# Optimization experiments

Measured on AMD Instinct MI355X. Metric: run time of the kernel, lower is better.

The kernel has to match this reference:

```python
import jax, jax.numpy as jnp
import numpy as np

N_NODES = 50000
N_EDGES = 800000
IN_F = 128
OUT_F = 128
EDGE_F = 6


def setup_inputs() -> dict:
    key = jax.random.key(0)
    k1, k2, k3, k4, k5, k6, k7 = jax.random.split(key, 7)
    nodeFeatures = jax.random.normal(k1, (N_NODES, IN_F), dtype=jnp.float32)
    edgeIndex = jax.random.randint(k2, (N_EDGES, 2), 0, N_NODES, dtype=jnp.int64)
    edgeFeatures = jax.random.normal(k3, (N_EDGES, EDGE_F), dtype=jnp.float32)
    # nn.Linear params (kaiming-uniform-ish init scale)
    lim_n = 1.0 / np.sqrt(IN_F)
    lim_e = 1.0 / np.sqrt(EDGE_F)
    W = jax.random.uniform(k4, (IN_F, OUT_F), minval=-lim_n, maxval=lim_n, dtype=jnp.float32)
    b = jax.random.uniform(k5, (OUT_F,), minval=-lim_n, maxval=lim_n, dtype=jnp.float32)
    We = jax.random.uniform(k6, (EDGE_F, OUT_F), minval=-lim_e, maxval=lim_e, dtype=jnp.float32)
    be = jax.random.uniform(k7, (OUT_F,), minval=-lim_e, maxval=lim_e, dtype=jnp.float32)
    return {"nodeFeatures": nodeFeatures, "edgeIndex": edgeIndex,
            "edgeFeatures": edgeFeatures, "W": W, "b": b, "We": We, "be": be}


def reference(nodeFeatures, edgeIndex, edgeFeatures, W, b, We, be):
    # node linear: [N, out]
    transformed = nodeFeatures @ W + b
    # edge linear: [E, out]
    edgeMsg = edgeFeatures @ We + be
    src = edgeIndex[:, 0]
    dst = edgeIndex[:, 1]
    # per-edge message = transformed[src] + edgeMsg, scatter-add into dst
    messages = transformed[src] + edgeMsg  # [E, out]
    aggregated = jax.ops.segment_sum(messages, dst, num_segments=nodeFeatures.shape[0])
    return jax.nn.relu(aggregated)
```

## Files before the change

### kernel.cpp

```cpp
#include <hip/hip_runtime.h>
#include <hip/hip_bf16.h>
#include <stdint.h>

#define IN_F 128
#define EDGE_F 6

using bf16x8 = __attribute__((ext_vector_type(8))) short;
using f32x4  = __attribute__((ext_vector_type(4))) float;

__device__ __forceinline__ float bf2f(unsigned short u) {
    return __uint_as_float(((unsigned int)u) << 16);
}
__device__ __forceinline__ unsigned short f2bfbits(float f) {
    __hip_bfloat16 h = __float2bfloat16(f);
    return *reinterpret_cast<unsigned short*>(&h);
}
__device__ __forceinline__ unsigned int packbf(float a, float b) {
    return ((unsigned int)f2bfbits(b) << 16) | (unsigned int)f2bfbits(a);
}

__global__ __launch_bounds__(256) void hist_cast(
        const int* __restrict__ eidx, const float* __restrict__ ef,
        int* __restrict__ cnt, int* __restrict__ rank,
        uint4* __restrict__ efp, int n_edges,
        const float* __restrict__ nf, unsigned short* __restrict__ nfb,
        int n_cast) {
    const int t = blockIdx.x * 256 + threadIdx.x;
    if (t < n_edges) {
        const int2 pr = reinterpret_cast<const int2*>(eidx)[t];
        const float2* efs = reinterpret_cast<const float2*>(ef + (size_t)t * EDGE_F);
        const float2 f0 = efs[0], f1 = efs[1], f2 = efs[2];
        uint4 q;
        q.x = (unsigned int)pr.x;
        q.y = packbf(f0.x, f0.y);
        q.z = packbf(f1.x, f1.y);
        q.w = packbf(f2.x, f2.y);
        efp[t] = q;
        rank[t] = atomicAdd(&cnt[pr.y], 1);
    }
    const int stride = gridDim.x * 256;
    for (int i = t; i < n_cast; i += stride) {
        const float4 lo = reinterpret_cast<const float4*>(nf)[2 * i];
        const float4 hi = reinterpret_cast<const float4*>(nf)[2 * i + 1];
        uint4 o;
        o.x = packbf(lo.x, lo.y); o.y = packbf(lo.z, lo.w);
        o.z = packbf(hi.x, hi.y); o.w = packbf(hi.z, hi.w);
        reinterpret_cast<uint4*>(nfb)[i] = o;
    }
}

__global__ __launch_bounds__(256) void scan_fused(
        const int* __restrict__ cnt, int* __restrict__ rowptr, int n, int nblk,
        unsigned long long* __restrict__ agg,
        const float* __restrict__ W, const float* __restrict__ b,
        const float* __restrict__ We, const float* __restrict__ be,
        unsigned short* __restrict__ Wpack, float* __restrict__ W2pack) {
    const int tid = threadIdx.x;
    const int blk = blockIdx.x;
    if (blk == nblk) {
        for (int idx = tid; idx < 16384; idx += 256) {
            int j = idx & 7, lane = (idx >> 3) & 63, ft = (idx >> 9) & 7, kb = idx >> 12;
            int k = kb * 32 + (lane >> 4) * 8 + j;
            int f = ft * 16 + (lane & 15);
            Wpack[idx] = f2bfbits(W[k * 128 + f]);
        }
        for (int idx = tid; idx < 1024; idx += 256) {
            int j = idx >> 7, f = idx & 127;
            float w = 0.f;
            if (j < 6)       w = We[j * 128 + f];
            else if (j == 6) w = b[f] + be[f];
            W2pack[idx] = w;
        }
        return;
    }
    __shared__ int sh[256];
    const int idx = blk * 256 + tid;
    const int v = (idx < n) ? cnt[idx] : 0;
    sh[tid] = v;
    __syncthreads();
    for (int off = 1; off < 256; off <<= 1) {
        int t2 = (tid >= off) ? sh[tid - off] : 0;
        __syncthreads();
        sh[tid] += t2;
        __syncthreads();
    }
    const int incl = sh[tid];
    if (tid == 0)
        atomicExch(&agg[blk], (1ULL << 32) | (unsigned int)sh[255]);
    int pre = 0;
    if (tid < blk) {
        unsigned long long x;
        do { x = atomicAdd(&agg[tid], 0ULL); } while ((x >> 32) == 0);
        pre = (int)(unsigned int)x;
    }
    __syncthreads();
    sh[tid] = pre;
    __syncthreads();
    for (int off = 128; off > 0; off >>= 1) {
        if (tid < off) sh[tid] += sh[tid + off];
        __syncthreads();
    }
    const int off0 = sh[0];
    if (idx < n) rowptr[idx] = off0 + incl - v;
    if (blk == nblk - 1 && tid == 255) rowptr[n] = off0 + incl;
}

__global__ __launch_bounds__(256) void fill_csr(
        const int* __restrict__ eidx, const int* __restrict__ rowptr,
        const int* __restrict__ rank, const uint4* __restrict__ efp,
        uint4* __restrict__ rec, int n_edges) {
    int e = blockIdx.x * 256 + threadIdx.x;
    if (e >= n_edges) return;
    const int dst = reinterpret_cast<const int2*>(eidx)[e].y;
    const int pos = rowptr[dst] + rank[e];
    rec[pos] = efp[e];
}

__global__ __launch_bounds__(256) void aggregate_bf16(
        const unsigned short* __restrict__ nfb, const uint4* __restrict__ rec,
        const int* __restrict__ rowptr, unsigned short* __restrict__ S,
        unsigned short* __restrict__ E8, int n_nodes) {
    const int lane = threadIdx.x & 63;
    const int wv = __builtin_amdgcn_readfirstlane(threadIdx.x >> 6);
    const int n = blockIdx.x * 4 + wv;
    if (n >= n_nodes) return;
    const int r0 = rowptr[n], r1 = rowptr[n + 1];
    const int deg = r1 - r0;
    float ax = 0.f, ay = 0.f;
    float e0 = 0.f, e1 = 0.f, e2 = 0.f, e3 = 0.f, e4 = 0.f, e5 = 0.f;
    int i = r0;
    for (; i + 7 < r1; i += 8) {
        uint4 q[8];
        unsigned int u[8];
#pragma unroll
        for (int j = 0; j < 8; ++j) q[j] = rec[i + j];
#pragma unroll
        for (int j = 0; j < 8; ++j)
            u[j] = reinterpret_cast<const unsigned int*>(nfb + (size_t)(int)q[j].x * IN_F)[lane];
#pragma unroll
        for (int j = 0; j < 8; ++j) {
            ax += bf2f((unsigned short)u[j]);
            ay += bf2f((unsigned short)(u[j] >> 16));
            e0 += bf2f((unsigned short)q[j].y);
            e1 += bf2f((unsigned short)(q[j].y >> 16));
            e2 += bf2f((unsigned short)q[j].z);
            e3 += bf2f((unsigned short)(q[j].z >> 16));
            e4 += bf2f((unsigned short)q[j].w);
            e5 += bf2f((unsigned short)(q[j].w >> 16));
        }
    }
    for (; i + 3 < r1; i += 4) {
        uint4 q[4];
        unsigned int u[4];
#pragma unroll
        for (int j = 0; j < 4; ++j) q[j] = rec[i + j];
#pragma unroll
        for (int j = 0; j < 4; ++j)
            u[j] = reinterpret_cast<const unsigned int*>(nfb + (size_t)(int)q[j].x * IN_F)[lane];
#pragma unroll
        for (int j = 0; j < 4; ++j) {
            ax += bf2f((unsigned short)u[j]);
            ay += bf2f((unsigned short)(u[j] >> 16));
            e0 += bf2f((unsigned short)q[j].y);
            e1 += bf2f((unsigned short)(q[j].y >> 16));
            e2 += bf2f((unsigned short)q[j].z);
            e3 += bf2f((unsigned short)(q[j].z >> 16));
            e4 += bf2f((unsigned short)q[j].w);
            e5 += bf2f((unsigned short)(q[j].w >> 16));
        }
    }
    for (; i < r1; ++i) {
        const uint4 q0 = rec[i];
        const unsigned int u0 = reinterpret_cast<const unsigned int*>(nfb + (size_t)(int)q0.x * IN_F)[lane];
        ax += bf2f((unsigned short)u0); ay += bf2f((unsigned short)(u0 >> 16));
        e0 += bf2f((unsigned short)q0.y); e1 += bf2f((unsigned short)(q0.y >> 16));
        e2 += bf2f((unsigned short)q0.z); e3 += bf2f((unsigned short)(q0.z >> 16));
        e4 += bf2f((unsigned short)q0.w); e5 += bf2f((unsigned short)(q0.w >> 16));
    }
    unsigned short* row = S + (size_t)n * IN_F;
    reinterpret_cast<unsigned int*>(row)[lane] = packbf(ax, ay);
    if (lane == 0) {
        uint4 q;
        q.x = packbf(e0, e1);
        q.y = packbf(e2, e3);
        q.z = packbf(e4, e5);
        q.w = packbf((float)deg, 0.f);
        *reinterpret_cast<uint4*>(E8 + (size_t)n * 8) = q;
    }
}

__global__ __launch_bounds__(256) void gemm_mfma(
        const unsigned short* __restrict__ S, const unsigned short* __restrict__ E8,
        const unsigned short* __restrict__ Wpack, const float* __restrict__ W2pack,
        float* __restrict__ out, int n_nodes) {
    __shared__ __align__(16) short Wl[16384];
    __shared__ float W2l[1024];
    const int tid = threadIdx.x;
    for (int i = tid; i < 2048; i += 256)
        reinterpret_cast<uint4*>(Wl)[i] = reinterpret_cast<const uint4*>(Wpack)[i];
    for (int i = tid; i < 1024; i += 256) W2l[i] = W2pack[i];

    const int wv = tid >> 6, lane = tid & 63;
    const int m = lane & 15, quad = lane >> 4;
    const int n0 = blockIdx.x * 64 + wv * 16;

    const int arow = min(n0 + m, n_nodes - 1);
    const unsigned short* ap = S + (size_t)arow * IN_F + quad * 8;
    bf16x8 a[4];
#pragma unroll
    for (int kb = 0; kb < 4; ++kb)
        a[kb] = *reinterpret_cast<const bf16x8*>(ap + kb * 32);

    __syncthreads();

    f32x4 acc[8];
#pragma unroll
    for (int ft = 0; ft < 8; ++ft) acc[ft] = (f32x4){0.f, 0.f, 0.f, 0.f};

#pragma unroll
    for (int kb = 0; kb < 4; ++kb) {
#pragma unroll
        for (int ft = 0; ft < 8; ++ft) {
            const bf16x8 bfrag =
                reinterpret_cast<const bf16x8*>(Wl)[(kb * 8 + ft) * 64 + lane];
            acc[ft] = __builtin_amdgcn_mfma_f32_16x16x32_bf16(a[kb], bfrag, acc[ft], 0, 0, 0);
        }
    }

    float e[4][7];
#pragma unroll
    for (int r = 0; r < 4; ++r) {
        const int n = min(n0 + quad * 4 + r, n_nodes - 1);
        const uint4 q = *reinterpret_cast<const uint4*>(E8 + (size_t)n * 8);
        e[r][0] = bf2f((unsigned short)q.x); e[r][1] = bf2f((unsigned short)(q.x >> 16));
        e[r][2] = bf2f((unsigned short)q.y); e[r][3] = bf2f((unsigned short)(q.y >> 16));
        e[r][4] = bf2f((unsigned short)q.z); e[r][5] = bf2f((unsigned short)(q.z >> 16));
        e[r][6] = bf2f((unsigned short)q.w);
    }
#pragma unroll
    for (int ft = 0; ft < 8; ++ft) {
        const int f = ft * 16 + m;
        float w2[7];
#pragma unroll
        for (int j = 0; j < 7; ++j) w2[j] = W2l[j * 128 + f];
#pragma unroll
        for (int r = 0; r < 4; ++r) {
            const int n = n0 + quad * 4 + r;
            if (n < n_nodes) {
                float v = acc[ft][r];
#pragma unroll
                for (int j = 0; j < 7; ++j) v += e[r][j] * w2[j];
                out[(size_t)n * 128 + f] = fmaxf(v, 0.f);
            }
        }
    }
}

extern "C" void kernel_launch(void* const* d_in, const int* in_sizes, int n_in,
                              void* d_out, int out_size, void* d_ws, size_t ws_size,
                              hipStream_t stream) {
    const float* nf = (const float*)d_in[0];
    const int* eidx = (const int*)d_in[1];
    const float* ef = (const float*)d_in[2];
    const float* W  = (const float*)d_in[3];
    const float* b  = (const float*)d_in[4];
    const float* We = (const float*)d_in[5];
    const float* be = (const float*)d_in[6];
    float* out = (float*)d_out;

    const int n_nodes = in_sizes[0] / IN_F;
    const int n_edges = in_sizes[1] / 2;

    uint4* rec = (uint4*)d_ws;
    uint4* efp = rec + n_edges;
    unsigned short* S = (unsigned short*)(efp + n_edges);
    unsigned short* E8 = S + (size_t)n_nodes * IN_F;
    unsigned short* Wpack = E8 + (size_t)n_nodes * 8;
    float* W2pack = (float*)(Wpack + 16384);
    int* cnt = (int*)(W2pack + 1024);
    unsigned long long* agg = (unsigned long long*)(cnt + n_nodes);
    int* rowptr = (int*)(agg + 256);
    int* rank   = rowptr + n_nodes + 1;
    unsigned short* nfb = (unsigned short*)(rank + n_edges);

    hipMemsetAsync(cnt, 0, (size_t)n_nodes * 4 + 256 * 8, stream);

    const int eb = (n_edges + 255) / 256;
    const int nblk = (n_nodes + 255) / 256;
    const int n_cast = n_nodes * (IN_F / 8);

    hist_cast<<<eb, 256, 0, stream>>>(eidx, ef, cnt, rank, efp, n_edges, nf, nfb, n_cast);
    scan_fused<<<nblk + 1, 256, 0, stream>>>(cnt, rowptr, n_nodes, nblk, agg,
                                             W, b, We, be, Wpack, W2pack);
    fill_csr<<<eb, 256, 0, stream>>>(eidx, rowptr, rank, efp, rec, n_edges);

    aggregate_bf16<<<(n_nodes + 3) / 4, 256, 0, stream>>>(nfb, rec, rowptr, S, E8, n_nodes);
    gemm_mfma<<<(n_nodes + 63) / 64, 256, 0, stream>>>(S, E8, Wpack, W2pack, out, n_nodes);
}
```

Before: 211.2 us.

## Replace global-atomic CSR build with two-level shared-memory counting sort

Builds the destination-sorted edge list with a coarse per-tile histogram over 256-node bins, a coarse scatter using shared-memory atomics, then a per-bin fine ranking that writes rowptr and the final records. It removes the global atomic histogram, the memset, the rank array and the decoupled-lookback scan. Source and destination are packed into 16 bits each in one word, which limits node count to 65536. The cost is an extra pass through an intermediate buffer.

Result: faster. 194.2 us (-8.0%).

```diff
diff --git a/kernel.cpp b/kernel.cpp
--- a/kernel.cpp
+++ b/kernel.cpp
@@ -4,6 +4,8 @@
 
 #define IN_F 128
 #define EDGE_F 6
+#define TILE_E 4096
+#define NBIN_PAD 256
 
 using bf16x8 = __attribute__((ext_vector_type(8))) short;
 using f32x4  = __attribute__((ext_vector_type(4))) float;
@@ -19,25 +21,65 @@
     return ((unsigned int)f2bfbits(b) << 16) | (unsigned int)f2bfbits(a);
 }
 
-__global__ __launch_bounds__(256) void hist_cast(
+__global__ __launch_bounds__(256) void pack_hist_cast(
         const int* __restrict__ eidx, const float* __restrict__ ef,
-        int* __restrict__ cnt, int* __restrict__ rank,
-        uint4* __restrict__ efp, int n_edges,
+        uint4* __restrict__ efp, unsigned short* __restrict__ pmat,
+        int n_edges, int nblk_e, int n_cast, int eb,
         const float* __restrict__ nf, unsigned short* __restrict__ nfb,
-        int n_cast) {
-    const int t = blockIdx.x * 256 + threadIdx.x;
-    if (t < n_edges) {
-        const int2 pr = reinterpret_cast<const int2*>(eidx)[t];
-        const float2* efs = reinterpret_cast<const float2*>(ef + (size_t)t * EDGE_F);
-        const float2 f0 = efs[0], f1 = efs[1], f2 = efs[2];
-        uint4 q;
-        q.x = (unsigned int)pr.x;
-        q.y = packbf(f0.x, f0.y);
-        q.z = packbf(f1.x, f1.y);
-        q.w = packbf(f2.x, f2.y);
-        efp[t] = q;
-        rank[t] = atomicAdd(&cnt[pr.y], 1);
-    }
+        const float* __restrict__ W, const float* __restrict__ b,
+        const float* __restrict__ We, const float* __restrict__ be,
+        unsigned short* __restrict__ Wpack, float* __restrict__ W2pack) {
+    const int tid = threadIdx.x;
+    const int blk = blockIdx.x;
+    __shared__ int hist[NBIN_PAD];
+
+    if (blk == eb) {
+        for (int idx = tid; idx < 16384; idx += 256) {
+            int j = idx & 7, lane = (idx >> 3) & 63, ft = (idx >> 9) & 7, kb = idx >> 12;
+            int k = kb * 32 + (lane >> 4) * 8 + j;
+            int f = ft * 16 + (lane & 15);
+            Wpack[idx] = f2bfbits(W[k * 128 + f]);
+        }
+        for (int idx = tid; idx < 1024; idx += 256) {
+            int j = idx >> 7, f = idx & 127;
+            float w = 0.f;
+            if (j < 6)       w = We[j * 128 + f];
+            else if (j == 6) w = b[f] + be[f];
+            W2pack[idx] = w;
+        }
+    } else {
+        const bool hb = (blk < nblk_e);
+        if (hb) {
+            hist[tid] = 0;
+            __syncthreads();
+        }
+        const int t = blk * 256 + tid;
+        if (t < n_edges) {
+            const int2 pr = reinterpret_cast<const int2*>(eidx)[t];
+            const float2* efs = reinterpret_cast<const float2*>(ef + (size_t)t * EDGE_F);
+            const float2 f0 = efs[0], f1 = efs[1], f2 = efs[2];
+            uint4 q;
+            q.x = (unsigned int)pr.x | ((unsigned int)pr.y << 16);
+            q.y = packbf(f0.x, f0.y);
+            q.z = packbf(f1.x, f1.y);
+            q.w = packbf(f2.x, f2.y);
+            efp[t] = q;
+        }
+        if (hb) {
+            const int e0 = blk * TILE_E;
+#pragma unroll
+            for (int i = 0; i < TILE_E / 256; ++i) {
+                const int e = e0 + i * 256 + tid;
+                if (e < n_edges) {
+                    const int dst = reinterpret_cast<const int2*>(eidx)[e].y;
+                    atomicAdd(&hist[dst >> 8], 1);
+                }
+            }
+            __syncthreads();
+            pmat[(size_t)blk * NBIN_PAD + tid] = (unsigned short)hist[tid];
+        }
+    }
+    const int t = blk * 256 + tid;
     const int stride = gridDim.x * 256;
     for (int i = t; i < n_cast; i += stride) {
         const float4 lo = reinterpret_cast<const float4*>(nf)[2 * i];
@@ -49,71 +91,79 @@
     }
 }
 
-__global__ __launch_bounds__(256) void scan_fused(
-        const int* __restrict__ cnt, int* __restrict__ rowptr, int n, int nblk,
-        unsigned long long* __restrict__ agg,
-        const float* __restrict__ W, const float* __restrict__ b,
-        const float* __restrict__ We, const float* __restrict__ be,
-        unsigned short* __restrict__ Wpack, float* __restrict__ W2pack) {
+__global__ __launch_bounds__(256) void coarse_scatter(
+        const uint4* __restrict__ efp, const unsigned short* __restrict__ pmat,
+        uint4* __restrict__ rec_c, int* __restrict__ gbase,
+        int n_edges, int nblk_e, int nbin) {
     const int tid = threadIdx.x;
     const int blk = blockIdx.x;
-    if (blk == nblk) {
-        for (int idx = tid; idx < 16384; idx += 256) {
-            int j = idx & 7, lane = (idx >> 3) & 63, ft = (idx >> 9) & 7, kb = idx >> 12;
-            int k = kb * 32 + (lane >> 4) * 8 + j;
-            int f = ft * 16 + (lane & 15);
-            Wpack[idx] = f2bfbits(W[k * 128 + f]);
-        }
-        for (int idx = tid; idx < 1024; idx += 256) {
-            int j = idx >> 7, f = idx & 127;
-            float w = 0.f;
-            if (j < 6)       w = We[j * 128 + f];
-            else if (j == 6) w = b[f] + be[f];
-            W2pack[idx] = w;
-        }
-        return;
-    }
-    __shared__ int sh[256];
-    const int idx = blk * 256 + tid;
-    const int v = (idx < n) ? cnt[idx] : 0;
-    sh[tid] = v;
+    __shared__ int cur[NBIN_PAD];
+    __shared__ int sc[NBIN_PAD];
+    int tot = 0, pre = 0;
+#pragma unroll 4
+    for (int bb = 0; bb < nblk_e; ++bb) {
+        const int v = pmat[(size_t)bb * NBIN_PAD + tid];
+        tot += v;
+        pre += (bb < blk) ? v : 0;
+    }
+    sc[tid] = tot;
     __syncthreads();
     for (int off = 1; off < 256; off <<= 1) {
-        int t2 = (tid >= off) ? sh[tid - off] : 0;
+        int t2 = (tid >= off) ? sc[tid - off] : 0;
         __syncthreads();
-        sh[tid] += t2;
+        sc[tid] += t2;
         __syncthreads();
     }
-    const int incl = sh[tid];
-    if (tid == 0)
-        atomicExch(&agg[blk], (1ULL << 32) | (unsigned int)sh[255]);
-    int pre = 0;
-    if (tid < blk) {
-        unsigned long long x;
-        do { x = atomicAdd(&agg[tid], 0ULL); } while ((x >> 32) == 0);
-        pre = (int)(unsigned int)x;
-    }
-    __syncthreads();
-    sh[tid] = pre;
-    __syncthreads();
-    for (int off = 128; off > 0; off >>= 1) {
-        if (tid < off) sh[tid] += sh[tid + off];
+    const int excl = sc[tid] - tot;
+    cur[tid] = excl + pre;
+    if (blk == 0 && tid <= nbin) gbase[tid] = excl;
+    __syncthreads();
+    const int e0 = blk * TILE_E;
+#pragma unroll
+    for (int i = 0; i < TILE_E / 256; ++i) {
+        const int e = e0 + i * 256 + tid;
+        if (e < n_edges) {
+            const uint4 q = efp[e];
+            const int cb = q.x >> 24;
+            const int pos = atomicAdd(&cur[cb], 1);
+            rec_c[pos] = q;
+        }
+    }
+}
+
+__global__ __launch_bounds__(256) void fine_rank(
+        const uint4* __restrict__ rec_c, const int* __restrict__ gbase,
+        uint4* __restrict__ rec, int* __restrict__ rowptr, int n_nodes) {
+    const int tid = threadIdx.x;
+    const int c = blockIdx.x;
+    const int rbase = gbase[c], rend = gbase[c + 1];
+    __shared__ int fcnt[256];
+    __shared__ int fpos[256];
+    fcnt[tid] = 0;
+    __syncthreads();
+    for (int i = rbase + tid; i < rend; i += 256) {
+        const unsigned int qx = reinterpret_cast<const unsigned int*>(rec_c)[(size_t)i * 4];
+        atomicAdd(&fcnt[(qx >> 16) & 255], 1);
+    }
+    __syncthreads();
+    const int own = fcnt[tid];
+    for (int off = 1; off < 256; off <<= 1) {
+        int t2 = (tid >= off) ? fcnt[tid - off] : 0;
         __syncthreads();
-    }
-    const int off0 = sh[0];
-    if (idx < n) rowptr[idx] = off0 + incl - v;
-    if (blk == nblk - 1 && tid == 255) rowptr[n] = off0 + incl;
-}
-
-__global__ __launch_bounds__(256) void fill_csr(
-        const int* __restrict__ eidx, const int* __restrict__ rowptr,
-        const int* __restrict__ rank, const uint4* __restrict__ efp,
-        uint4* __restrict__ rec, int n_edges) {
-    int e = blockIdx.x * 256 + threadIdx.x;
-    if (e >= n_edges) return;
-    const int dst = reinterpret_cast<const int2*>(eidx)[e].y;
-    const int pos = rowptr[dst] + rank[e];
-    rec[pos] = efp[e];
+        fcnt[tid] += t2;
+        __syncthreads();
+    }
+    const int excl = fcnt[tid] - own;
+    fpos[tid] = excl;
+    const int n = c * 256 + tid;
+    if (n <= n_nodes) rowptr[n] = rbase + excl;
+    if (c == 0 && tid == 0) rowptr[n_nodes] = gbase[gridDim.x];
+    __syncthreads();
+    for (int i = rbase + tid; i < rend; i += 256) {
+        const uint4 q = rec_c[i];
+        const int r = atomicAdd(&fpos[(q.x >> 16) & 255], 1);
+        rec[rbase + r] = q;
+    }
 }
 
 __global__ __launch_bounds__(256) void aggregate_bf16(
@@ -136,7 +186,7 @@
         for (int j = 0; j < 8; ++j) q[j] = rec[i + j];
 #pragma unroll
         for (int j = 0; j < 8; ++j)
-            u[j] = reinterpret_cast<const unsigned int*>(nfb + (size_t)(int)q[j].x * IN_F)[lane];
+            u[j] = reinterpret_cast<const unsigned int*>(nfb + (size_t)(q[j].x & 0xFFFFu) * IN_F)[lane];
 #pragma unroll
         for (int j = 0; j < 8; ++j) {
             ax += bf2f((unsigned short)u[j]);
@@ -156,7 +206,7 @@
         for (int j = 0; j < 4; ++j) q[j] = rec[i + j];
 #pragma unroll
         for (int j = 0; j < 4; ++j)
-            u[j] = reinterpret_cast<const unsigned int*>(nfb + (size_t)(int)q[j].x * IN_F)[lane];
+            u[j] = reinterpret_cast<const unsigned int*>(nfb + (size_t)(q[j].x & 0xFFFFu) * IN_F)[lane];
 #pragma unroll
         for (int j = 0; j < 4; ++j) {
             ax += bf2f((unsigned short)u[j]);
@@ -171,7 +221,7 @@
     }
     for (; i < r1; ++i) {
         const uint4 q0 = rec[i];
-        const unsigned int u0 = reinterpret_cast<const unsigned int*>(nfb + (size_t)(int)q0.x * IN_F)[lane];
+        const unsigned int u0 = reinterpret_cast<const unsigned int*>(nfb + (size_t)(q0.x & 0xFFFFu) * IN_F)[lane];
         ax += bf2f((unsigned short)u0); ay += bf2f((unsigned short)(u0 >> 16));
         e0 += bf2f((unsigned short)q0.y); e1 += bf2f((unsigned short)(q0.y >> 16));
         e2 += bf2f((unsigned short)q0.z); e3 += bf2f((unsigned short)(q0.z >> 16));
@@ -271,29 +321,30 @@
     const int n_nodes = in_sizes[0] / IN_F;
     const int n_edges = in_sizes[1] / 2;
 
-    uint4* rec = (uint4*)d_ws;
-    uint4* efp = rec + n_edges;
-    unsigned short* S = (unsigned short*)(efp + n_edges);
+    const int eb = (n_edges + 255) / 256;
+    const int nblk_e = (n_edges + TILE_E - 1) / TILE_E;
+    const int nbin = (n_nodes + 255) >> 8;
+    const int n_cast = n_nodes * (IN_F / 8);
+
+    uint4* rec   = (uint4*)d_ws;
+    uint4* efp   = rec + n_edges;
+    uint4* rec_c = efp + n_edges;
+    unsigned short* S = (unsigned short*)(rec_c + n_edges);
     unsigned short* E8 = S + (size_t)n_nodes * IN_F;
     unsigned short* Wpack = E8 + (size_t)n_nodes * 8;
     float* W2pack = (float*)(Wpack + 16384);
-    int* cnt = (int*)(W2pack + 1024);
-    unsigned long long* agg = (unsigned long long*)(cnt + n_nodes);
-    int* rowptr = (int*)(agg + 256);
-    int* rank   = rowptr + n_nodes + 1;
-    unsigned short* nfb = (unsigned short*)(rank + n_edges);
-
-    hipMemsetAsync(cnt, 0, (size_t)n_nodes * 4 + 256 * 8, stream);
-
-    const int eb = (n_edges + 255) / 256;
-    const int nblk = (n_nodes + 255) / 256;
-    const int n_cast = n_nodes * (IN_F / 8);
-
-    hist_cast<<<eb, 256, 0, stream>>>(eidx, ef, cnt, rank, efp, n_edges, nf, nfb, n_cast);
-    scan_fused<<<nblk + 1, 256, 0, stream>>>(cnt, rowptr, n_nodes, nblk, agg,
-                                             W, b, We, be, Wpack, W2pack);
-    fill_csr<<<eb, 256, 0, stream>>>(eidx, rowptr, rank, efp, rec, n_edges);
-
+    unsigned short* pmat = (unsigned short*)(W2pack + 1024);
+    int* gbase  = (int*)(pmat + (size_t)nblk_e * NBIN_PAD);
+    int* rowptr = gbase + 260;
+    const int rp_pad = (n_nodes + 1 + 3) & ~3;
+    unsigned short* nfb = (unsigned short*)(rowptr + rp_pad);
+
+    pack_hist_cast<<<eb + 1, 256, 0, stream>>>(eidx, ef, efp, pmat,
+                                               n_edges, nblk_e, n_cast, eb,
+                                               nf, nfb, W, b, We, be, Wpack, W2pack);
+    coarse_scatter<<<nblk_e, 256, 0, stream>>>(efp, pmat, rec_c, gbase,
+                                               n_edges, nblk_e, nbin);
+    fine_rank<<<nbin, 256, 0, stream>>>(rec_c, gbase, rec, rowptr, n_nodes);
     aggregate_bf16<<<(n_nodes + 3) / 4, 256, 0, stream>>>(nfb, rec, rowptr, S, E8, n_nodes);
     gemm_mfma<<<(n_nodes + 63) / 64, 256, 0, stream>>>(S, E8, Wpack, W2pack, out, n_nodes);
 }
```
